# Kernel tuning notes

Hardware: AMD Instinct MI355X
Metric: run time of the kernel (lower is better)

## Reference

```python
import jax, jax.numpy as jnp
import numpy as np
import math

D_MODEL = 1024
NUM_HEADS = 16
D_K = D_MODEL // NUM_HEADS
NUM_BUCKETS = 32
MAX_DISTANCE = 512  # PositionalEncoding max_len


def _relative_position_bucket(relative_position):
    # Faithful to the torch code: both signs add num_buckets//2 (==16), rp==0 adds 0.
    half = NUM_BUCKETS // 2            # 16
    max_exact = NUM_BUCKETS // 4       # 8
    base = (relative_position > 0).astype(jnp.int32) * half \
         + (relative_position < 0).astype(jnp.int32) * half
    arp = jnp.abs(relative_position)
    is_small = arp < max_exact
    safe = jnp.maximum(arp, 1).astype(jnp.float32)  # avoid log(0); masked by is_small anyway
    large = max_exact + (jnp.log(safe / max_exact)
                         / math.log(MAX_DISTANCE / max_exact)
                         * (half - max_exact)).astype(jnp.int32)  # trunc == torch .long()
    large = jnp.minimum(large, half - 1)
    return base + jnp.where(is_small, arp, large)


def compute_bias(rel_bias_table, seq_length):
    ctx = jnp.arange(seq_length, dtype=jnp.int32)[:, None]
    mem = jnp.arange(seq_length, dtype=jnp.int32)[None, :]
    buckets = _relative_position_bucket(mem - ctx)        # [S, S]
    values = rel_bias_table[buckets]                       # [S, S, H]
    return jnp.transpose(values, (2, 0, 1))[None]          # [1, H, S, S]


def setup_inputs() -> dict:
    key = jax.random.key(0)
    ks = jax.random.split(key, 12)
    B, S, D = 2, 2048, D_MODEL
    scale = 1.0 / math.sqrt(D)
    inp = {
        "query": jax.random.normal(ks[0], (B, S, D), jnp.float32),
        "key": jax.random.normal(ks[1], (B, S, D), jnp.float32),
        "value": jax.random.normal(ks[2], (B, S, D), jnp.float32),
        "Wq": jax.random.normal(ks[3], (D, D), jnp.float32) * scale,
        "bq": jnp.zeros((D,), jnp.float32),
        "Wk": jax.random.normal(ks[4], (D, D), jnp.float32) * scale,
        "bk": jnp.zeros((D,), jnp.float32),
        "Wv": jax.random.normal(ks[5], (D, D), jnp.float32) * scale,
        "bv": jnp.zeros((D,), jnp.float32),
        "Wo": jax.random.normal(ks[6], (D, D), jnp.float32) * scale,
        "bo": jnp.zeros((D,), jnp.float32),
        "rel_bias_table": jax.random.normal(ks[7], (NUM_BUCKETS, NUM_HEADS), jnp.float32) * 0.1,
    }
    return inp


def reference(query, key, value, Wq, bq, Wk, bk, Wv, bv, Wo, bo, rel_bias_table):
    B, Sq, D = query.shape
    Sk = key.shape[1]
    H, dk = NUM_HEADS, D_K
    q = (query @ Wq + bq).reshape(B, Sq, H, dk)
    k = (key @ Wk + bk).reshape(B, Sk, H, dk)
    v = (value @ Wv + bv).reshape(B, Sk, H, dk)
    scores = jnp.einsum('bqhd,bkhd->bhqk', q, k) / math.sqrt(dk)  # [B,H,Sq,Sk]
    position_bias = compute_bias(rel_bias_table, max(Sq, Sk))[:, :, :Sq, :Sk]
    scores = scores + position_bias  # broadcast over batch (torch expand)
    attn_weights = jax.nn.softmax(scores, axis=-1)
    # dropout is identity in eval / p=0
    context = jnp.einsum('bhqk,bkhd->bqhd', attn_weights, v).reshape(B, Sq, D)
    output = context @ Wo + bo
    pb = jnp.broadcast_to(position_bias, (B, H, Sq, Sk))
    return output, attn_weights, pb
```

## Files before the change

kernel.cpp:

```cpp
#include <hip/hip_runtime.h>
#include <hip/hip_bf16.h>

#define BN 2
#define SEQ 2048
#define DM 1024
#define NH 16
#define DK 64

using f32x4  = __attribute__((ext_vector_type(4))) float;
using bf16x8 = __attribute__((ext_vector_type(8))) __bf16;
using short8 = __attribute__((ext_vector_type(8))) short;

static_assert(sizeof(bf16x8) == 16, "bf16x8 must be 16B");

#define MFMA16(a, b, c) __builtin_amdgcn_mfma_f32_16x16x32_bf16(a, b, c, 0, 0, 0)

__device__ __forceinline__ unsigned short f2b(float f) {
    __hip_bfloat16 h = __float2bfloat16(f);
    return __builtin_bit_cast(unsigned short, h);
}

__device__ __forceinline__ bf16x8 load_bf8(const unsigned short* p) {
    short8 s = *reinterpret_cast<const short8*>(p);
    return __builtin_bit_cast(bf16x8, s);
}

__global__ void bias_table_kernel(const float* __restrict__ rel,
                                  float* __restrict__ bias_val) {
    int idx = blockIdx.x * 256 + threadIdx.x;
    if (idx >= NH * 4095) return;
    int h = idx / 4095;
    int dd = idx - h * 4095;
    int d = dd - 2047;
    int a = d < 0 ? -d : d;
    int bucket;
    if (a == 0) bucket = 0;
    else if (a < 8) bucket = 16 + a;
    else {
        int k = (a >= 14) + (a >= 23) + (a >= 39) + (a >= 64) +
                (a >= 108) + (a >= 182) + (a >= 305);
        bucket = 24 + k;
    }
    bias_val[h * 4095 + dd] = rel[bucket * NH + h];
}

__global__ __launch_bounds__(256) void wtrans_kernel(
        const float* __restrict__ W0, const float* __restrict__ W1,
        const float* __restrict__ W2, const float* __restrict__ W3,
        unsigned short* __restrict__ T0, unsigned short* __restrict__ T1,
        unsigned short* __restrict__ T2, unsigned short* __restrict__ T3) {
    constexpr int P = 68;
    __shared__ unsigned short lt[64 * P];
    const int mz = blockIdx.z;
    const float* W = mz == 0 ? W0 : mz == 1 ? W1 : mz == 2 ? W2 : W3;
    unsigned short* T = mz == 0 ? T0 : mz == 1 ? T1 : mz == 2 ? T2 : T3;
    const int k0 = blockIdx.x * 64, n0 = blockIdx.y * 64;
    const int tid = threadIdx.x;
#pragma unroll
    for (int p = 0; p < 4; ++p) {
        int r = p * 16 + (tid >> 4);
        int c = (tid & 15) * 4;
        float4 vv = *(const float4*)&W[(size_t)(k0 + r) * DM + n0 + c];
#pragma unroll
        for (int j = 0; j < 4; ++j) {
            int n = c + j;
            float x = j == 0 ? vv.x : j == 1 ? vv.y : j == 2 ? vv.z : vv.w;
            lt[n * P + (r ^ ((n & 7) << 3))] = f2b(x);
        }
    }
    __syncthreads();
#pragma unroll
    for (int p = 0; p < 2; ++p) {
        int rn = p * 32 + (tid >> 3);
        int ck = (tid & 7) * 8;
        int ckx = ck ^ ((rn & 7) << 3);
        ushort4 a0 = *(ushort4*)&lt[rn * P + ckx];
        ushort4 a1 = *(ushort4*)&lt[rn * P + ckx + 4];
        *(ushort4*)&T[(size_t)(n0 + rn) * DM + k0 + ck] = a0;
        *(ushort4*)&T[(size_t)(n0 + rn) * DM + k0 + ck + 4] = a1;
    }
}

__global__ __launch_bounds__(256) void qkv_gemm(
        const float* __restrict__ Aq, const float* __restrict__ Ak, const float* __restrict__ Av,
        const unsigned short* __restrict__ Wtq, const unsigned short* __restrict__ Wtk,
        const unsigned short* __restrict__ Wtv,
        const float* __restrict__ bq, const float* __restrict__ bk, const float* __restrict__ bv,
        unsigned short* __restrict__ Qp, unsigned short* __restrict__ Kh,
        unsigned short* __restrict__ Vt) {
    constexpr int KP = 40;
    __shared__ unsigned short la[128 * KP];
    __shared__ unsigned short lb[128 * KP];
    const int mat = blockIdx.z;
    const float* A = mat == 0 ? Aq : mat == 1 ? Ak : Av;
    const unsigned short* Wt = mat == 0 ? Wtq : mat == 1 ? Wtk : Wtv;
    const float* bias = mat == 0 ? bq : mat == 1 ? bk : bv;
    const float outscale = mat == 0 ? 0.125f : 1.0f;
    const int tid = threadIdx.x;
    const int m0 = blockIdx.y * 128, n0 = blockIdx.x * 128;
    const int lane = tid & 63, wid = tid >> 6;
    const int wm0 = (wid >> 1) * 64, wn0 = (wid & 1) * 64;
    const int l15 = lane & 15, l4 = lane >> 4;
    f32x4 acc[4][4] = {};

    for (int kt = 0; kt < 32; ++kt) {
        const int k0 = kt * 32;
#pragma unroll
        for (int i = 0; i < 4; ++i) {
            int idx = tid + i * 256;
            int row = idx >> 3, c4 = (idx & 7) * 4;
            float4 v = *(const float4*)(A + (size_t)(m0 + row) * DM + k0 + c4);
            ushort4 u; u.x = f2b(v.x); u.y = f2b(v.y); u.z = f2b(v.z); u.w = f2b(v.w);
            *(ushort4*)&la[row * KP + c4] = u;
        }
#pragma unroll
        for (int i = 0; i < 2; ++i) {
            int idx = tid + i * 256;
            int row = idx >> 2, c8 = (idx & 3) * 8;
            *(int4*)&lb[row * KP + c8] =
                *(const int4*)&Wt[(size_t)(n0 + row) * DM + k0 + c8];
        }
        __syncthreads();
        bf16x8 af[4], bfv[4];
#pragma unroll
        for (int m = 0; m < 4; ++m)
            af[m] = load_bf8(&la[(wm0 + m * 16 + l15) * KP + l4 * 8]);
#pragma unroll
        for (int n = 0; n < 4; ++n)
            bfv[n] = load_bf8(&lb[(wn0 + n * 16 + l15) * KP + l4 * 8]);
#pragma unroll
        for (int m = 0; m < 4; ++m)
#pragma unroll
            for (int n = 0; n < 4; ++n)
                acc[m][n] = MFMA16(af[m], bfv[n], acc[m][n]);
        __syncthreads();
    }

    float bv4[4];
#pragma unroll
    for (int n = 0; n < 4; ++n) bv4[n] = bias[n0 + wn0 + n * 16 + l15];
#pragma unroll
    for (int m = 0; m < 4; ++m) {
#pragma unroll
        for (int n = 0; n < 4; ++n) {
            int gcol = n0 + wn0 + n * 16 + l15;
#pragma unroll
            for (int r = 0; r < 4; ++r) {
                int grow = m0 + wm0 + m * 16 + l4 * 4 + r;
                float val = (acc[m][n][r] + bv4[n]) * outscale;
                unsigned short ob = f2b(val);
                int b = grow >> 11, s = grow & 2047;
                int hh = gcol >> 6, dl = gcol & 63;
                if (mat == 0) {
                    Qp[(size_t)grow * DM + gcol] = ob;
                } else if (mat == 1) {
                    Kh[(((size_t)(b * NH + hh) * SEQ + s) << 6) + dl] = ob;
                } else {
                    Vt[(((size_t)(b * NH + hh) * DK + dl) << 11) + s] = ob;
                }
            }
        }
    }
}

__global__ __launch_bounds__(256) void o_gemm(
        const unsigned short* __restrict__ Actx, const unsigned short* __restrict__ Wto,
        const float* __restrict__ bo, float* __restrict__ out) {
    constexpr int KP = 40;
    __shared__ unsigned short la[64 * KP];
    __shared__ unsigned short lb[128 * KP];
    const int tid = threadIdx.x;
    const int m0 = blockIdx.y * 64, n0 = blockIdx.x * 128;
    const int lane = tid & 63, wid = tid >> 6;
    const int wm0 = (wid >> 1) * 32, wn0 = (wid & 1) * 64;
    const int l15 = lane & 15, l4 = lane >> 4;
    f32x4 acc[2][4] = {};

    for (int kt = 0; kt < 32; ++kt) {
        const int k0 = kt * 32;
        {
            int row = tid >> 2, c8 = (tid & 3) * 8;
            *(int4*)&la[row * KP + c8] =
                *(const int4*)&Actx[(size_t)(m0 + row) * DM + k0 + c8];
        }
#pragma unroll
        for (int i = 0; i < 2; ++i) {
            int idx = tid + i * 256;
            int row = idx >> 2, c8 = (idx & 3) * 8;
            *(int4*)&lb[row * KP + c8] =
                *(const int4*)&Wto[(size_t)(n0 + row) * DM + k0 + c8];
        }
        __syncthreads();
        bf16x8 af[2], bfv[4];
#pragma unroll
        for (int m = 0; m < 2; ++m)
            af[m] = load_bf8(&la[(wm0 + m * 16 + l15) * KP + l4 * 8]);
#pragma unroll
        for (int n = 0; n < 4; ++n)
            bfv[n] = load_bf8(&lb[(wn0 + n * 16 + l15) * KP + l4 * 8]);
#pragma unroll
        for (int m = 0; m < 2; ++m)
#pragma unroll
            for (int n = 0; n < 4; ++n)
                acc[m][n] = MFMA16(af[m], bfv[n], acc[m][n]);
        __syncthreads();
    }

#pragma unroll
    for (int m = 0; m < 2; ++m)
#pragma unroll
        for (int n = 0; n < 4; ++n) {
            int gcol = n0 + wn0 + n * 16 + l15;
            float bb = bo[gcol];
#pragma unroll
            for (int r = 0; r < 4; ++r) {
                int grow = m0 + wm0 + m * 16 + l4 * 4 + r;
                out[(size_t)grow * DM + gcol] = acc[m][n][r] + bb;
            }
        }
}

__global__ __launch_bounds__(256, 4) void attn11_kernel(
        const unsigned short* __restrict__ Qp, const unsigned short* __restrict__ Kh,
        const unsigned short* __restrict__ Vt, const float* __restrict__ bias_val,
        float* __restrict__ attn_out, float* __restrict__ pb_out,
        unsigned short* __restrict__ ctx) {
    __shared__ float bias_lds[2112];
    __shared__ float wtile[2][4][16 * 36];
    const int tid = threadIdx.x;
    const int lane = tid & 63, wid = tid >> 6;
    const int l15 = lane & 15, l4 = lane >> 4;
    const int bid = (blockIdx.x & 7) * 128 + (blockIdx.x >> 3);
    const int qb = bid & 31;
    const int h = (bid >> 5) & 15;
    const int b = bid >> 9;
    const int q0 = qb * 64;
    const int qw = q0 + wid * 16;

    {
        const float* bp = bias_val + h * 4095 + (2047 - (q0 + 63));
        for (int i = tid; i < 2111; i += 256) bias_lds[i] = bp[i];
    }
    __syncthreads();

    const unsigned short* qbase = Qp + (size_t)(b * SEQ + qw + l15) * DM + h * DK;
    bf16x8 qa0 = load_bf8(qbase + l4 * 8);
    bf16x8 qa1 = load_bf8(qbase + 32 + l4 * 8);

    const unsigned short* kbase = Kh + (((size_t)(b * NH + h) * SEQ) << 6);
    const int bbase = 63 - wid * 16 - l4 * 4;

    float m[4], l[4];
#pragma unroll
    for (int r = 0; r < 4; ++r) { m[r] = -3e38f; l[r] = 0.f; }

    for (int c0 = 0; c0 < SEQ; c0 += 32) {
        const unsigned short* kp = kbase + ((size_t)(c0 + l15) << 6);
        bf16x8 k00 = load_bf8(kp + l4 * 8);
        bf16x8 k01 = load_bf8(kp + 32 + l4 * 8);
        bf16x8 k10 = load_bf8(kp + (16 << 6) + l4 * 8);
        bf16x8 k11 = load_bf8(kp + (16 << 6) + 32 + l4 * 8);
        f32x4 a0 = {}, a1 = {};
        a0 = MFMA16(qa0, k00, a0); a0 = MFMA16(qa1, k01, a0);
        a1 = MFMA16(qa0, k10, a1); a1 = MFMA16(qa1, k11, a1);
#pragma unroll
        for (int r = 0; r < 4; ++r) {
            float s0 = a0[r] + bias_lds[c0 + l15 + bbase - r];
            float s1 = a1[r] + bias_lds[c0 + 16 + l15 + bbase - r];
            float cm = fmaxf(s0, s1);
            if (cm > m[r]) { l[r] *= __expf(m[r] - cm); m[r] = cm; }
            l[r] += __expf(s0 - m[r]) + __expf(s1 - m[r]);
        }
    }
#pragma unroll
    for (int off = 1; off < 16; off <<= 1) {
#pragma unroll
        for (int r = 0; r < 4; ++r) {
            float om = __shfl_xor(m[r], off);
            float ol = __shfl_xor(l[r], off);
            float M = fmaxf(m[r], om);
            l[r] = l[r] * __expf(m[r] - M) + ol * __expf(om - M);
            m[r] = M;
        }
    }
    float invl[4];
#pragma unroll
    for (int r = 0; r < 4; ++r) invl[r] = 1.0f / l[r];

    float* abase = attn_out + ((size_t)((b * NH + h) * SEQ + qw)) * SEQ;
    float* pbase = pb_out + ((size_t)((b * NH + h) * SEQ + qw)) * SEQ;
    const unsigned short* vbase = Vt + (((size_t)(b * NH + h) * DK) << 11);
    f32x4 cacc[4] = {};

    bf16x8 k00, k01, k10, k11;
    {
        const unsigned short* kp = kbase + ((size_t)l15 << 6);
        k00 = load_bf8(kp + l4 * 8);
        k01 = load_bf8(kp + 32 + l4 * 8);
        k10 = load_bf8(kp + (16 << 6) + l4 * 8);
        k11 = load_bf8(kp + (16 << 6) + 32 + l4 * 8);
    }
    const int srow = lane >> 2, scg = (lane & 3) * 8;
    int cur = 0;
    for (int c0 = 0; c0 < SEQ; c0 += 32, cur ^= 1) {
        f32x4 a0 = {}, a1 = {};
        a0 = MFMA16(qa0, k00, a0); a0 = MFMA16(qa1, k01, a0);
        a1 = MFMA16(qa0, k10, a1); a1 = MFMA16(qa1, k11, a1);
        const int cn = (c0 + 32) & (SEQ - 1);
        const unsigned short* kp = kbase + ((size_t)(cn + l15) << 6);
        k00 = load_bf8(kp + l4 * 8);
        k01 = load_bf8(kp + 32 + l4 * 8);
        k10 = load_bf8(kp + (16 << 6) + l4 * 8);
        k11 = load_bf8(kp + (16 << 6) + 32 + l4 * 8);
        bf16x8 vv0 = load_bf8(vbase + ((size_t)(0 * 16 + l15) << 11) + c0 + l4 * 8);
        bf16x8 vv1 = load_bf8(vbase + ((size_t)(1 * 16 + l15) << 11) + c0 + l4 * 8);
        bf16x8 vv2 = load_bf8(vbase + ((size_t)(2 * 16 + l15) << 11) + c0 + l4 * 8);
        bf16x8 vv3 = load_bf8(vbase + ((size_t)(3 * 16 + l15) << 11) + c0 + l4 * 8);
        float* wt = wtile[cur][wid];
#pragma unroll
        for (int r = 0; r < 4; ++r) {
            int row = l4 * 4 + r;
            float b0 = bias_lds[c0 + l15 + bbase - r];
            float b1 = bias_lds[c0 + 16 + l15 + bbase - r];
            float w0 = __expf(a0[r] + b0 - m[r]) * invl[r];
            float w1 = __expf(a1[r] + b1 - m[r]) * invl[r];
            wt[row * 36 + l15] = w0;
            wt[row * 36 + 16 + l15] = w1;
            float* gp = pbase + (size_t)row * SEQ + c0 + l15;
            gp[0] = b0;
            gp[16] = b1;
        }
        asm volatile("s_waitcnt lgkmcnt(0)" ::: "memory");
        __builtin_amdgcn_sched_barrier(0);
        {
            float4 v0 = *(const float4*)&wt[srow * 36 + scg];
            float4 v1 = *(const float4*)&wt[srow * 36 + scg + 4];
            float* gp = abase + (size_t)srow * SEQ + c0 + scg;
            *(float4*)gp = v0;
            *(float4*)(gp + 4) = v1;
        }
        float4 pA = *(const float4*)&wt[l15 * 36 + l4 * 8];
        float4 pB = *(const float4*)&wt[l15 * 36 + l4 * 8 + 4];
        short8 ps;
        ps[0] = (short)f2b(pA.x); ps[1] = (short)f2b(pA.y);
        ps[2] = (short)f2b(pA.z); ps[3] = (short)f2b(pA.w);
        ps[4] = (short)f2b(pB.x); ps[5] = (short)f2b(pB.y);
        ps[6] = (short)f2b(pB.z); ps[7] = (short)f2b(pB.w);
        bf16x8 pf = __builtin_bit_cast(bf16x8, ps);
        cacc[0] = MFMA16(pf, vv0, cacc[0]);
        cacc[1] = MFMA16(pf, vv1, cacc[1]);
        cacc[2] = MFMA16(pf, vv2, cacc[2]);
        cacc[3] = MFMA16(pf, vv3, cacc[3]);
    }
#pragma unroll
    for (int d0 = 0; d0 < 4; ++d0)
#pragma unroll
        for (int r = 0; r < 4; ++r)
            ctx[(size_t)(b * SEQ + qw + l4 * 4 + r) * DM + h * DK + d0 * 16 + l15] =
                f2b(cacc[d0][r]);
}

extern "C" void kernel_launch(void* const* d_in, const int* in_sizes, int n_in,
                              void* d_out, int out_size, void* d_ws, size_t ws_size,
                              hipStream_t stream) {
    const float* query = (const float*)d_in[0];
    const float* key   = (const float*)d_in[1];
    const float* value = (const float*)d_in[2];
    const float* Wq = (const float*)d_in[3];
    const float* bq = (const float*)d_in[4];
    const float* Wk = (const float*)d_in[5];
    const float* bk = (const float*)d_in[6];
    const float* Wv = (const float*)d_in[7];
    const float* bv = (const float*)d_in[8];
    const float* Wo = (const float*)d_in[9];
    const float* bo = (const float*)d_in[10];
    const float* rel = (const float*)d_in[11];

    float* out = (float*)d_out;
    float* attn_out = out + (size_t)BN * SEQ * DM;
    float* pb_out = attn_out + (size_t)BN * NH * SEQ * SEQ;

    char* ws = (char*)d_ws;
    float* bias_val = (float*)ws;
    unsigned short* Qp  = (unsigned short*)(ws + 262144);
    unsigned short* Kh  = Qp + (size_t)BN * SEQ * DM;
    unsigned short* Vt  = Kh + (size_t)BN * SEQ * DM;
    unsigned short* ctx = Vt + (size_t)BN * SEQ * DM;
    unsigned short* Wtq = ctx + (size_t)BN * SEQ * DM;
    unsigned short* Wtk = Wtq + (size_t)DM * DM;
    unsigned short* Wtv = Wtk + (size_t)DM * DM;
    unsigned short* Wto = Wtv + (size_t)DM * DM;

    bias_table_kernel<<<256, 256, 0, stream>>>(rel, bias_val);
    wtrans_kernel<<<dim3(16, 16, 4), 256, 0, stream>>>(Wq, Wk, Wv, Wo, Wtq, Wtk, Wtv, Wto);
    qkv_gemm<<<dim3(8, 32, 3), 256, 0, stream>>>(query, key, value, Wtq, Wtk, Wtv,
                                                 bq, bk, bv, Qp, Kh, Vt);
    attn11_kernel<<<BN * NH * (SEQ / 64), 256, 0, stream>>>(Qp, Kh, Vt, bias_val,
                                                            attn_out, pb_out, ctx);
    o_gemm<<<dim3(8, 64), 256, 0, stream>>>(ctx, Wto, bo, out);
}
```

Measured before the change: 597.9 us.

## Pre-convert activations to bf16 and stage GEMM tiles via async global-to-LDS loads

Adds a separate kernel that converts the fp32 query/key/value inputs to bf16. It stores them in the pb_out output region as scratch before the attention kernel overwrites it. The QKV and output-projection GEMMs now fill their shared-memory tiles with direct global_load_lds 16-byte transfers instead of register round trips, using an unpadded 32-element row stride. This removes per-tile conversion and register staging from the GEMM loops, at the cost of an extra pass over the inputs and possible LDS bank conflicts from dropping the padding.

```diff
diff --git a/kernel.cpp b/kernel.cpp
--- a/kernel.cpp
+++ b/kernel.cpp
@@ -23,6 +23,12 @@
 __device__ __forceinline__ bf16x8 load_bf8(const unsigned short* p) {
     short8 s = *reinterpret_cast<const short8*>(p);
     return __builtin_bit_cast(bf16x8, s);
+}
+
+__device__ __forceinline__ void async16(unsigned short* l, const unsigned short* g) {
+    __builtin_amdgcn_global_load_lds(
+        (const __attribute__((address_space(1))) unsigned int*)g,
+        (__attribute__((address_space(3))) unsigned int*)l, 16, 0, 0);
 }
 
 __global__ void bias_table_kernel(const float* __restrict__ rel,
@@ -44,6 +50,24 @@
     bias_val[h * 4095 + dd] = rel[bucket * NH + h];
 }
 
+__global__ __launch_bounds__(256) void conv_bf16(
+        const float* __restrict__ Xq, const float* __restrict__ Xk,
+        const float* __restrict__ Xv,
+        unsigned short* __restrict__ Yq, unsigned short* __restrict__ Yk,
+        unsigned short* __restrict__ Yv) {
+    const int z = blockIdx.y;
+    const float* X = z == 0 ? Xq : z == 1 ? Xk : Xv;
+    unsigned short* Y = z == 0 ? Yq : z == 1 ? Yk : Yv;
+    int i = (blockIdx.x * 256 + threadIdx.x) * 8;
+    float4 a = *(const float4*)(X + i);
+    float4 b = *(const float4*)(X + i + 4);
+    ushort4 u0, u1;
+    u0.x = f2b(a.x); u0.y = f2b(a.y); u0.z = f2b(a.z); u0.w = f2b(a.w);
+    u1.x = f2b(b.x); u1.y = f2b(b.y); u1.z = f2b(b.z); u1.w = f2b(b.w);
+    *(ushort4*)(Y + i) = u0;
+    *(ushort4*)(Y + i + 4) = u1;
+}
+
 __global__ __launch_bounds__(256) void wtrans_kernel(
         const float* __restrict__ W0, const float* __restrict__ W1,
         const float* __restrict__ W2, const float* __restrict__ W3,
@@ -81,18 +105,18 @@
     }
 }
 
-__global__ __launch_bounds__(256) void qkv_gemm(
-        const float* __restrict__ Aq, const float* __restrict__ Ak, const float* __restrict__ Av,
+__global__ __launch_bounds__(256) void qkv_gemm2(
+        const unsigned short* __restrict__ Ab0, const unsigned short* __restrict__ Ab1,
+        const unsigned short* __restrict__ Ab2,
         const unsigned short* __restrict__ Wtq, const unsigned short* __restrict__ Wtk,
         const unsigned short* __restrict__ Wtv,
         const float* __restrict__ bq, const float* __restrict__ bk, const float* __restrict__ bv,
         unsigned short* __restrict__ Qp, unsigned short* __restrict__ Kh,
         unsigned short* __restrict__ Vt) {
-    constexpr int KP = 40;
-    __shared__ unsigned short la[128 * KP];
-    __shared__ unsigned short lb[128 * KP];
+    __shared__ unsigned short la[128 * 32];
+    __shared__ unsigned short lb[128 * 32];
     const int mat = blockIdx.z;
-    const float* A = mat == 0 ? Aq : mat == 1 ? Ak : Av;
+    const unsigned short* A = mat == 0 ? Ab0 : mat == 1 ? Ab1 : Ab2;
     const unsigned short* Wt = mat == 0 ? Wtq : mat == 1 ? Wtk : Wtv;
     const float* bias = mat == 0 ? bq : mat == 1 ? bk : bv;
     const float outscale = mat == 0 ? 0.125f : 1.0f;
@@ -106,28 +130,21 @@
     for (int kt = 0; kt < 32; ++kt) {
         const int k0 = kt * 32;
 #pragma unroll
-        for (int i = 0; i < 4; ++i) {
-            int idx = tid + i * 256;
-            int row = idx >> 3, c4 = (idx & 7) * 4;
-            float4 v = *(const float4*)(A + (size_t)(m0 + row) * DM + k0 + c4);
-            ushort4 u; u.x = f2b(v.x); u.y = f2b(v.y); u.z = f2b(v.z); u.w = f2b(v.w);
-            *(ushort4*)&la[row * KP + c4] = u;
-        }
-#pragma unroll
         for (int i = 0; i < 2; ++i) {
-            int idx = tid + i * 256;
-            int row = idx >> 2, c8 = (idx & 3) * 8;
-            *(int4*)&lb[row * KP + c8] =
-                *(const int4*)&Wt[(size_t)(n0 + row) * DM + k0 + c8];
+            const int chb = i * 256 + wid * 64;
+            const int ch = chb + lane;
+            const int row = ch >> 2, sg = (ch & 3) * 8;
+            async16(&la[chb * 8], A + (size_t)(m0 + row) * DM + k0 + sg);
+            async16(&lb[chb * 8], Wt + (size_t)(n0 + row) * DM + k0 + sg);
         }
         __syncthreads();
         bf16x8 af[4], bfv[4];
 #pragma unroll
         for (int m = 0; m < 4; ++m)
-            af[m] = load_bf8(&la[(wm0 + m * 16 + l15) * KP + l4 * 8]);
+            af[m] = load_bf8(&la[(wm0 + m * 16 + l15) * 32 + l4 * 8]);
 #pragma unroll
         for (int n = 0; n < 4; ++n)
-            bfv[n] = load_bf8(&lb[(wn0 + n * 16 + l15) * KP + l4 * 8]);
+            bfv[n] = load_bf8(&lb[(wn0 + n * 16 + l15) * 32 + l4 * 8]);
 #pragma unroll
         for (int m = 0; m < 4; ++m)
 #pragma unroll
@@ -163,12 +180,11 @@
     }
 }
 
-__global__ __launch_bounds__(256) void o_gemm(
+__global__ __launch_bounds__(256) void o_gemm2(
         const unsigned short* __restrict__ Actx, const unsigned short* __restrict__ Wto,
         const float* __restrict__ bo, float* __restrict__ out) {
-    constexpr int KP = 40;
-    __shared__ unsigned short la[64 * KP];
-    __shared__ unsigned short lb[128 * KP];
+    __shared__ unsigned short la[64 * 32];
+    __shared__ unsigned short lb[128 * 32];
     const int tid = threadIdx.x;
     const int m0 = blockIdx.y * 64, n0 = blockIdx.x * 128;
     const int lane = tid & 63, wid = tid >> 6;
@@ -179,25 +195,26 @@
     for (int kt = 0; kt < 32; ++kt) {
         const int k0 = kt * 32;
         {
-            int row = tid >> 2, c8 = (tid & 3) * 8;
-            *(int4*)&la[row * KP + c8] =
-                *(const int4*)&Actx[(size_t)(m0 + row) * DM + k0 + c8];
+            const int chb = wid * 64;
+            const int ch = chb + lane;
+            const int row = ch >> 2, sg = (ch & 3) * 8;
+            async16(&la[chb * 8], Actx + (size_t)(m0 + row) * DM + k0 + sg);
         }
 #pragma unroll
         for (int i = 0; i < 2; ++i) {
-            int idx = tid + i * 256;
-            int row = idx >> 2, c8 = (idx & 3) * 8;
-            *(int4*)&lb[row * KP + c8] =
-                *(const int4*)&Wto[(size_t)(n0 + row) * DM + k0 + c8];
+            const int chb = i * 256 + wid * 64;
+            const int ch = chb + lane;
+            const int row = ch >> 2, sg = (ch & 3) * 8;
+            async16(&lb[chb * 8], Wto + (size_t)(n0 + row) * DM + k0 + sg);
         }
         __syncthreads();
         bf16x8 af[2], bfv[4];
 #pragma unroll
         for (int m = 0; m < 2; ++m)
-            af[m] = load_bf8(&la[(wm0 + m * 16 + l15) * KP + l4 * 8]);
+            af[m] = load_bf8(&la[(wm0 + m * 16 + l15) * 32 + l4 * 8]);
 #pragma unroll
         for (int n = 0; n < 4; ++n)
-            bfv[n] = load_bf8(&lb[(wn0 + n * 16 + l15) * KP + l4 * 8]);
+            bfv[n] = load_bf8(&lb[(wn0 + n * 16 + l15) * 32 + l4 * 8]);
 #pragma unroll
         for (int m = 0; m < 2; ++m)
 #pragma unroll
@@ -220,7 +237,7 @@
         }
 }
 
-__global__ __launch_bounds__(256, 4) void attn11_kernel(
+__global__ __launch_bounds__(256, 4) void attn13_kernel(
         const unsigned short* __restrict__ Qp, const unsigned short* __restrict__ Kh,
         const unsigned short* __restrict__ Vt, const float* __restrict__ bias_val,
         float* __restrict__ attn_out, float* __restrict__ pb_out,
@@ -391,11 +408,16 @@
     unsigned short* Wtv = Wtk + (size_t)DM * DM;
     unsigned short* Wto = Wtv + (size_t)DM * DM;
 
+    unsigned short* Qb = (unsigned short*)pb_out;
+    unsigned short* Kb = Qb + (size_t)BN * SEQ * DM;
+    unsigned short* Vb = Kb + (size_t)BN * SEQ * DM;
+
     bias_table_kernel<<<256, 256, 0, stream>>>(rel, bias_val);
     wtrans_kernel<<<dim3(16, 16, 4), 256, 0, stream>>>(Wq, Wk, Wv, Wo, Wtq, Wtk, Wtv, Wto);
-    qkv_gemm<<<dim3(8, 32, 3), 256, 0, stream>>>(query, key, value, Wtq, Wtk, Wtv,
-                                                 bq, bk, bv, Qp, Kh, Vt);
-    attn11_kernel<<<BN * NH * (SEQ / 64), 256, 0, stream>>>(Qp, Kh, Vt, bias_val,
+    conv_bf16<<<dim3(2048, 3), 256, 0, stream>>>(query, key, value, Qb, Kb, Vb);
+    qkv_gemm2<<<dim3(8, 32, 3), 256, 0, stream>>>(Qb, Kb, Vb, Wtq, Wtk, Wtv,
+                                                  bq, bk, bv, Qp, Kh, Vt);
+    attn13_kernel<<<BN * NH * (SEQ / 64), 256, 0, stream>>>(Qp, Kh, Vt, bias_val,
                                                             attn_out, pb_out, ctx);
-    o_gemm<<<dim3(8, 64), 256, 0, stream>>>(ctx, Wto, bo, out);
-}
+    o_gemm2<<<dim3(8, 64), 256, 0, stream>>>(ctx, Wto, bo, out);
+}
```

New measurement: 600.2 us. Within noise of the previous version (+0.4%).
